# Kernel tuning notes

Hardware: AMD Instinct MI355X
Metric: run time of the kernel (lower is better)

Reference implementation:

```python
import jax, jax.numpy as jnp
import numpy as np

N_NODES = 50000


def _gcn_norm(edge_index, n):
    # Add self-loops (PyG GCNConv default) and compute symmetric normalization.
    src = jnp.concatenate([edge_index[0], jnp.arange(n, dtype=edge_index.dtype)])
    dst = jnp.concatenate([edge_index[1], jnp.arange(n, dtype=edge_index.dtype)])
    deg = jax.ops.segment_sum(jnp.ones(src.shape[0], dtype=jnp.float32), dst,
                              num_segments=n)
    dinv = jnp.where(deg > 0, jax.lax.rsqrt(deg), 0.0)
    norm = dinv[src] * dinv[dst]  # [E+N]
    return src, dst, norm


def _gcn_conv(x, src, dst, norm, W, b, n):
    h = x @ W                              # [N, out] linear transform first
    msgs = h[src] * norm[:, None]          # gather + edge-wise scale [E+N, out]
    out = jax.ops.segment_sum(msgs, dst, num_segments=n)  # scatter-add
    return out + b


def setup_inputs() -> dict:
    key = jax.random.key(0)
    k1, k2, k3, k4 = jax.random.split(key, 4)
    N, E, F, H, C = N_NODES, 1600000, 128, 128, 64
    x = jax.random.normal(k1, (N, F), dtype=jnp.float32)
    edge_index = jax.random.randint(k2, (2, E), 0, N, dtype=jnp.int64)
    W1 = jax.random.normal(k3, (F, H), dtype=jnp.float32) * 0.05
    b1 = jnp.zeros((H,), dtype=jnp.float32)
    W2 = jax.random.normal(k4, (H, C), dtype=jnp.float32) * 0.05
    b2 = jnp.zeros((C,), dtype=jnp.float32)
    return {"x": x, "edge_index": edge_index, "W1": W1, "b1": b1,
            "W2": W2, "b2": b2}


def reference(x, edge_index, W1, b1, W2, b2):
    n = x.shape[0]
    src, dst, norm = _gcn_norm(edge_index, n)
    h = _gcn_conv(x, src, dst, norm, W1, b1, n)
    h = jax.nn.relu(h)
    out = _gcn_conv(h, src, dst, norm, W2, b2, n)
    return out
```

## Files before the change

kernel.cpp:

```cpp
#include <hip/hip_runtime.h>
#include <hip/hip_bf16.h>
#include <stdint.h>

#define N_NODES 50000
#define N_EDGES 1600000
#define N_TOT   (N_EDGES + N_NODES)
#define NBKT      256
#define BKT_NODES 196
#define BKT_CAP   7168
#define TILE      4096
#define EPT       16

typedef unsigned short u16;
typedef __attribute__((ext_vector_type(8))) short short8;
typedef __attribute__((ext_vector_type(4))) float floatx4;

__device__ __forceinline__ float b2f(u16 u) {
    union { unsigned int i; float f; } v; v.i = ((unsigned int)u) << 16; return v.f;
}
__device__ __forceinline__ u16 f2b(float f) {
    union { unsigned int i; float f; } v; v.f = f;
    unsigned int r = (v.i + 0x7FFFu + ((v.i >> 16) & 1u)) >> 16;
    return (u16)r;
}

__global__ void k_detect(const unsigned* __restrict__ xw,
                         const unsigned* __restrict__ ew,
                         int* __restrict__ flags) {
    __shared__ int cnt[2];
    int tid = threadIdx.x;
    if (tid < 2) cnt[tid] = 0;
    __syncthreads();
    unsigned w = xw[tid];
    int e = (w >> 7) & 0xFF;
    int plaus = (e == 0) || (e >= 0x60 && e <= 0x9F);
    unsigned hw = ew[2 * tid + 1];
    atomicAdd(&cnt[0], plaus);
    atomicAdd(&cnt[1], hw == 0 ? 1 : 0);
    __syncthreads();
    if (tid == 0) {
        flags[0] = (cnt[0] < 160) ? 1 : 0;
        flags[1] = (cnt[1] > 250) ? 1 : 0;
    }
}

__global__ void k_zero(int* p) { p[threadIdx.x] = 0; }

__global__ __launch_bounds__(256) void k_part(const int* __restrict__ ei,
                                              const int* __restrict__ flags,
                                              unsigned* __restrict__ pairs,
                                              int* __restrict__ bktcnt) {
    __shared__ unsigned pairsL[TILE];
    __shared__ unsigned char bktL[TILE];
    __shared__ int hist[NBKT], incl[NBKT], delta[NBKT];
    int tid = threadIdx.x;
    long base = (long)blockIdx.x * TILE;
    int i64 = flags[1];
    hist[tid] = 0;
    __syncthreads();

    int myb[EPT], myrank[EPT]; unsigned myp[EPT];
#pragma unroll
    for (int t = 0; t < EPT; t++) {
        long idx = base + t * 256 + tid;
        int b = -1; unsigned p = 0;
        if (idx < N_TOT) {
            int s, d;
            if (idx < N_EDGES) {
                if (i64) { s = ei[2 * idx]; d = ei[2 * (N_EDGES + idx)]; }
                else     { s = ei[idx];     d = ei[N_EDGES + idx]; }
            } else {
                s = d = (int)(idx - N_EDGES);
            }
            b = d / BKT_NODES;
            p = (unsigned)s | ((unsigned)(d - b * BKT_NODES) << 16);
        }
        myb[t] = b; myp[t] = p;
        myrank[t] = (b >= 0) ? atomicAdd(&hist[b], 1) : 0;
    }
    __syncthreads();

    int tot = hist[tid];
    incl[tid] = tot;
    __syncthreads();
    for (int o = 1; o < NBKT; o <<= 1) {
        int t2 = (tid >= o) ? incl[tid - o] : 0;
        __syncthreads();
        incl[tid] += t2;
        __syncthreads();
    }
    int excl = incl[tid] - tot;
    int gb = atomicAdd(&bktcnt[tid], tot);
    hist[tid]  = excl;
    delta[tid] = tid * BKT_CAP + gb - excl;
    __syncthreads();

#pragma unroll
    for (int t = 0; t < EPT; t++) {
        if (myb[t] >= 0) {
            int slot = hist[myb[t]] + myrank[t];
            pairsL[slot] = myp[t];
            bktL[slot]   = (unsigned char)myb[t];
        }
    }
    __syncthreads();
    int count = incl[NBKT - 1];
    for (int i = tid; i < count; i += 256) {
        int b = bktL[i];
        int pos = delta[b] + i;
        if (pos - b * BKT_CAP < BKT_CAP)
            pairs[pos] = pairsL[i];
    }
}

__global__ __launch_bounds__(256) void k_bktscan(const int* __restrict__ bktcnt,
                                                 int* __restrict__ bktbase) {
    __shared__ int s[NBKT];
    int tid = threadIdx.x;
    int v = bktcnt[tid];
    s[tid] = v;
    __syncthreads();
    for (int o = 1; o < NBKT; o <<= 1) {
        int t = (tid >= o) ? s[tid - o] : 0;
        __syncthreads();
        s[tid] += t;
        __syncthreads();
    }
    bktbase[tid] = s[tid] - v;
}

__global__ __launch_bounds__(256) void k_bucket(const unsigned* __restrict__ pairs,
                                                const int* __restrict__ bktcnt,
                                                const int* __restrict__ bktbase,
                                                int* __restrict__ rowstart,
                                                int* __restrict__ deg,
                                                float* __restrict__ dinv,
                                                u16* __restrict__ csr) {
    __shared__ u16 csrL[BKT_CAP];
    __shared__ int degL[NBKT], curL[NBKT], scanT[NBKT];
    int b = blockIdx.x, tid = threadIdx.x;
    int cnt  = bktcnt[b];
    int base = bktbase[b];
    const unsigned* reg = pairs + (size_t)b * BKT_CAP;
    degL[tid] = 0;
    __syncthreads();
    for (int i = tid; i < cnt; i += 256)
        atomicAdd(&degL[reg[i] >> 16], 1);
    __syncthreads();
    int v = degL[tid];
    scanT[tid] = v;
    __syncthreads();
    for (int o = 1; o < NBKT; o <<= 1) {
        int t = (tid >= o) ? scanT[tid - o] : 0;
        __syncthreads();
        scanT[tid] += t;
        __syncthreads();
    }
    int excl = scanT[tid] - v;
    curL[tid] = excl;
    int n = b * BKT_NODES + tid;
    if (tid < BKT_NODES && n < N_NODES) {
        rowstart[n] = base + excl;
        deg[n]      = v;
        dinv[n]     = rsqrtf((float)v);
    }
    __syncthreads();
    for (int i = tid; i < cnt; i += 256) {
        unsigned p = reg[i];
        int slot = atomicAdd(&curL[p >> 16], 1);
        csrL[slot] = (u16)(p & 0xFFFFu);
    }
    __syncthreads();
    for (int i = tid; i < cnt; i += 256)
        csr[base + i] = csrL[i];
}

template<int NOUT, bool ADYN>
__global__ __launch_bounds__(256) void k_gemm(const void* __restrict__ A,
                                              const void* __restrict__ W,
                                              u16* __restrict__ out, int M,
                                              const int* __restrict__ flags) {
    const int isf32 = flags[0];
    constexpr int LDW = 136;
    __shared__ __align__(16) u16 Wt[NOUT * LDW];
    int tid = threadIdx.x;
    const float* Wf = (const float*)W;
    const u16*   Wu = (const u16*)W;
    for (int idx = tid; idx < 128 * NOUT; idx += 256) {
        int k = idx / NOUT, n = idx % NOUT;
        Wt[n * LDW + k] = isf32 ? f2b(Wf[idx]) : Wu[idx];
    }
    __syncthreads();

    int wave = tid >> 6, lane = tid & 63;
    int quad = lane >> 4, l16 = lane & 15;
    int r0 = blockIdx.x * 64 + wave * 16;
    int r = r0 + l16; if (r >= M) r = M - 1;

    floatx4 acc[NOUT / 16];
#pragma unroll
    for (int i = 0; i < NOUT / 16; i++) acc[i] = (floatx4)(0.f);

#pragma unroll
    for (int ks = 0; ks < 4; ks++) {
        short8 a;
        if (ADYN && isf32) {
            const float* af = (const float*)A + (size_t)r * 128 + ks * 32 + quad * 8;
            float4 v0 = ((const float4*)af)[0];
            float4 v1 = ((const float4*)af)[1];
            a[0] = (short)f2b(v0.x); a[1] = (short)f2b(v0.y);
            a[2] = (short)f2b(v0.z); a[3] = (short)f2b(v0.w);
            a[4] = (short)f2b(v1.x); a[5] = (short)f2b(v1.y);
            a[6] = (short)f2b(v1.z); a[7] = (short)f2b(v1.w);
        } else {
            a = ((const short8*)((const u16*)A + (size_t)r * 128))[ks * 4 + quad];
        }
#pragma unroll
        for (int nt = 0; nt < NOUT / 16; nt++) {
            const short8* bp = (const short8*)&Wt[(nt * 16 + l16) * LDW + ks * 32 + quad * 8];
            acc[nt] = __builtin_amdgcn_mfma_f32_16x16x32_bf16(a, *bp, acc[nt], 0, 0, 0);
        }
    }
#pragma unroll
    for (int nt = 0; nt < NOUT / 16; nt++) {
#pragma unroll
        for (int j = 0; j < 4; j++) {
            int row = r0 + quad * 4 + j;
            if (row < M) out[(size_t)row * NOUT + nt * 16 + l16] = f2b(acc[nt][j]);
        }
    }
}

__global__ __launch_bounds__(256) void k_agg1(const u16* __restrict__ h,
                                              const u16* __restrict__ csr,
                                              const int* __restrict__ rowstart,
                                              const int* __restrict__ deg,
                                              const float* __restrict__ dinv,
                                              const void* __restrict__ bias,
                                              u16* __restrict__ out,
                                              const int* __restrict__ flags) {
    int wave = threadIdx.x >> 6, lane = threadIdx.x & 63;
    int d = blockIdx.x * 4 + wave;
    if (d >= N_NODES) return;
    int quad = lane >> 4, l16 = lane & 15;
    int start = rowstart[d], end = start + deg[d];
    float dd = dinv[d];
    float acc[8] = {0.f, 0.f, 0.f, 0.f, 0.f, 0.f, 0.f, 0.f};
    for (int e = start + quad; e < end; e += 4) {
        int s = csr[e];
        float w = dinv[s] * dd;
        uint4 v = ((const uint4*)(h + (size_t)s * 128))[l16];
        acc[0] += w * b2f(v.x & 0xFFFF); acc[1] += w * b2f(v.x >> 16);
        acc[2] += w * b2f(v.y & 0xFFFF); acc[3] += w * b2f(v.y >> 16);
        acc[4] += w * b2f(v.z & 0xFFFF); acc[5] += w * b2f(v.z >> 16);
        acc[6] += w * b2f(v.w & 0xFFFF); acc[7] += w * b2f(v.w >> 16);
    }
#pragma unroll
    for (int j = 0; j < 8; j++) {
        acc[j] += __shfl_xor(acc[j], 16);
        acc[j] += __shfl_xor(acc[j], 32);
    }
    if (quad == 0) {
        int isf32 = flags[0];
        u16 r[8];
#pragma unroll
        for (int j = 0; j < 8; j++) {
            float bv = isf32 ? ((const float*)bias)[l16 * 8 + j]
                             : b2f(((const u16*)bias)[l16 * 8 + j]);
            float v = acc[j] + bv;
            r[j] = f2b(v > 0.f ? v : 0.f);
        }
        uint4 o;
        o.x = r[0] | ((unsigned)r[1] << 16); o.y = r[2] | ((unsigned)r[3] << 16);
        o.z = r[4] | ((unsigned)r[5] << 16); o.w = r[6] | ((unsigned)r[7] << 16);
        ((uint4*)(out + (size_t)d * 128))[l16] = o;
    }
}

__global__ __launch_bounds__(256) void k_agg2(const u16* __restrict__ h,
                                              const u16* __restrict__ csr,
                                              const int* __restrict__ rowstart,
                                              const int* __restrict__ deg,
                                              const float* __restrict__ dinv,
                                              const void* __restrict__ bias,
                                              float* __restrict__ out,
                                              const int* __restrict__ flags) {
    int wave = threadIdx.x >> 6, lane = threadIdx.x & 63;
    int d = blockIdx.x * 4 + wave;
    if (d >= N_NODES) return;
    int oct = lane >> 3, l8 = lane & 7;
    int start = rowstart[d], end = start + deg[d];
    float dd = dinv[d];
    float acc[8] = {0.f, 0.f, 0.f, 0.f, 0.f, 0.f, 0.f, 0.f};
    for (int e = start + oct; e < end; e += 8) {
        int s = csr[e];
        float w = dinv[s] * dd;
        uint4 v = ((const uint4*)(h + (size_t)s * 64))[l8];
        acc[0] += w * b2f(v.x & 0xFFFF); acc[1] += w * b2f(v.x >> 16);
        acc[2] += w * b2f(v.y & 0xFFFF); acc[3] += w * b2f(v.y >> 16);
        acc[4] += w * b2f(v.z & 0xFFFF); acc[5] += w * b2f(v.z >> 16);
        acc[6] += w * b2f(v.w & 0xFFFF); acc[7] += w * b2f(v.w >> 16);
    }
#pragma unroll
    for (int j = 0; j < 8; j++) {
        acc[j] += __shfl_xor(acc[j], 8);
        acc[j] += __shfl_xor(acc[j], 16);
        acc[j] += __shfl_xor(acc[j], 32);
    }
    if (oct == 0) {
        int isf32 = flags[0];
        float r[8];
#pragma unroll
        for (int j = 0; j < 8; j++) {
            float bv = isf32 ? ((const float*)bias)[l8 * 8 + j]
                             : b2f(((const u16*)bias)[l8 * 8 + j]);
            r[j] = acc[j] + bv;
        }
        float4 oa, ob;
        oa.x = r[0]; oa.y = r[1]; oa.z = r[2]; oa.w = r[3];
        ob.x = r[4]; ob.y = r[5]; ob.z = r[6]; ob.w = r[7];
        ((float4*)(out + (size_t)d * 64))[l8 * 2]     = oa;
        ((float4*)(out + (size_t)d * 64))[l8 * 2 + 1] = ob;
    }
}

extern "C" void kernel_launch(void* const* d_in, const int* in_sizes, int n_in,
                              void* d_out, int out_size, void* d_ws, size_t ws_size,
                              hipStream_t stream) {
    const void* x  = d_in[0];
    const int*  ei = (const int*)d_in[1];
    const void* W1 = d_in[2];
    const void* b1 = d_in[3];
    const void* W2 = d_in[4];
    const void* b2 = d_in[5];
    float* out = (float*)d_out;

    char* ws = (char*)d_ws;
    int*      flags    = (int*)(ws + 0);
    int*      bktcnt   = (int*)(ws + 1024);
    int*      bktbase  = (int*)(ws + 2048);
    int*      deg      = (int*)(ws + 4096);
    int*      rowstart = (int*)(ws + 204800);
    float*    dinv     = (float*)(ws + 405504);
    unsigned* pairs    = (unsigned*)(ws + 606208);
    u16*      csr      = (u16*)(ws + 7946240);
    u16*      h1       = (u16*)(ws + 11247616);
    u16*      out1     = (u16*)(ws + 24047616);
    u16*      h2       = h1;

    k_detect <<<1, 256, 0, stream>>>((const unsigned*)x, (const unsigned*)ei, flags);
    k_zero   <<<1, 256, 0, stream>>>(bktcnt);
    k_part   <<<(N_TOT + TILE - 1) / TILE, 256, 0, stream>>>(ei, flags, pairs, bktcnt);
    k_bktscan<<<1, 256, 0, stream>>>(bktcnt, bktbase);
    k_bucket <<<NBKT, 256, 0, stream>>>(pairs, bktcnt, bktbase, rowstart, deg, dinv, csr);

    k_gemm<128, true> <<<(N_NODES + 63) / 64, 256, 0, stream>>>(x, W1, h1, N_NODES, flags);
    k_agg1<<<(N_NODES + 3) / 4, 256, 0, stream>>>(h1, csr, rowstart, deg, dinv, b1, out1, flags);
    k_gemm<64, false> <<<(N_NODES + 63) / 64, 256, 0, stream>>>(out1, W2, h2, N_NODES, flags);
    k_agg2<<<(N_NODES + 3) / 4, 256, 0, stream>>>(h2, csr, rowstart, deg, dinv, b2, out, flags);
}
```

Baseline: 290.4 us.

## Fold source-degree scaling into GEMM epilogue and widen aggregation lanes

The GEMM epilogue now multiplies each output row by dinv[row], so the aggregation kernels no longer gather dinv[src] per edge. They apply the destination dinv once at the end instead. The aggregation kernels give each lane 16 features instead of 8, process two edges per iteration with more edges in flight, and reduce with an extra shuffle stage. The zero-init kernel is merged into the detect kernel to save one launch. This trades a per-edge random load and multiply for a slightly different rounding order, since the pre-scaled values are stored in bf16.

```diff
diff --git a/kernel.cpp b/kernel.cpp
--- a/kernel.cpp
+++ b/kernel.cpp
@@ -26,9 +26,11 @@
 
 __global__ void k_detect(const unsigned* __restrict__ xw,
                          const unsigned* __restrict__ ew,
-                         int* __restrict__ flags) {
+                         int* __restrict__ flags,
+                         int* __restrict__ bktcnt) {
     __shared__ int cnt[2];
     int tid = threadIdx.x;
+    bktcnt[tid] = 0;
     if (tid < 2) cnt[tid] = 0;
     __syncthreads();
     unsigned w = xw[tid];
@@ -43,8 +45,6 @@
         flags[1] = (cnt[1] > 250) ? 1 : 0;
     }
 }
-
-__global__ void k_zero(int* p) { p[threadIdx.x] = 0; }
 
 __global__ __launch_bounds__(256) void k_part(const int* __restrict__ ei,
                                               const int* __restrict__ flags,
@@ -178,6 +178,7 @@
 template<int NOUT, bool ADYN>
 __global__ __launch_bounds__(256) void k_gemm(const void* __restrict__ A,
                                               const void* __restrict__ W,
+                                              const float* __restrict__ dinv,
                                               u16* __restrict__ out, int M,
                                               const int* __restrict__ flags) {
     const int isf32 = flags[0];
@@ -221,12 +222,18 @@
             acc[nt] = __builtin_amdgcn_mfma_f32_16x16x32_bf16(a, *bp, acc[nt], 0, 0, 0);
         }
     }
+    float sc[4];
+#pragma unroll
+    for (int j = 0; j < 4; j++) {
+        int row = r0 + quad * 4 + j;
+        sc[j] = dinv[row < M ? row : 0];
+    }
 #pragma unroll
     for (int nt = 0; nt < NOUT / 16; nt++) {
 #pragma unroll
         for (int j = 0; j < 4; j++) {
             int row = r0 + quad * 4 + j;
-            if (row < M) out[(size_t)row * NOUT + nt * 16 + l16] = f2b(acc[nt][j]);
+            if (row < M) out[(size_t)row * NOUT + nt * 16 + l16] = f2b(acc[nt][j] * sc[j]);
         }
     }
 }
@@ -242,38 +249,73 @@
     int wave = threadIdx.x >> 6, lane = threadIdx.x & 63;
     int d = blockIdx.x * 4 + wave;
     if (d >= N_NODES) return;
-    int quad = lane >> 4, l16 = lane & 15;
+    int oct = lane >> 3, l8 = lane & 7;
     int start = rowstart[d], end = start + deg[d];
-    float dd = dinv[d];
-    float acc[8] = {0.f, 0.f, 0.f, 0.f, 0.f, 0.f, 0.f, 0.f};
-    for (int e = start + quad; e < end; e += 4) {
-        int s = csr[e];
-        float w = dinv[s] * dd;
-        uint4 v = ((const uint4*)(h + (size_t)s * 128))[l16];
-        acc[0] += w * b2f(v.x & 0xFFFF); acc[1] += w * b2f(v.x >> 16);
-        acc[2] += w * b2f(v.y & 0xFFFF); acc[3] += w * b2f(v.y >> 16);
-        acc[4] += w * b2f(v.z & 0xFFFF); acc[5] += w * b2f(v.z >> 16);
-        acc[6] += w * b2f(v.w & 0xFFFF); acc[7] += w * b2f(v.w >> 16);
-    }
-#pragma unroll
-    for (int j = 0; j < 8; j++) {
+    float acc[16];
+#pragma unroll
+    for (int j = 0; j < 16; j++) acc[j] = 0.f;
+
+    int e = start + oct;
+    for (; e + 8 < end; e += 16) {
+        int s0 = csr[e], s1 = csr[e + 8];
+        const uint4* p0 = (const uint4*)(h + (size_t)s0 * 128);
+        const uint4* p1 = (const uint4*)(h + (size_t)s1 * 128);
+        uint4 a0 = p0[l8 * 2], b0 = p0[l8 * 2 + 1];
+        uint4 a1 = p1[l8 * 2], b1 = p1[l8 * 2 + 1];
+        acc[0]  += b2f(a0.x & 0xFFFF); acc[1]  += b2f(a0.x >> 16);
+        acc[2]  += b2f(a0.y & 0xFFFF); acc[3]  += b2f(a0.y >> 16);
+        acc[4]  += b2f(a0.z & 0xFFFF); acc[5]  += b2f(a0.z >> 16);
+        acc[6]  += b2f(a0.w & 0xFFFF); acc[7]  += b2f(a0.w >> 16);
+        acc[8]  += b2f(b0.x & 0xFFFF); acc[9]  += b2f(b0.x >> 16);
+        acc[10] += b2f(b0.y & 0xFFFF); acc[11] += b2f(b0.y >> 16);
+        acc[12] += b2f(b0.z & 0xFFFF); acc[13] += b2f(b0.z >> 16);
+        acc[14] += b2f(b0.w & 0xFFFF); acc[15] += b2f(b0.w >> 16);
+        acc[0]  += b2f(a1.x & 0xFFFF); acc[1]  += b2f(a1.x >> 16);
+        acc[2]  += b2f(a1.y & 0xFFFF); acc[3]  += b2f(a1.y >> 16);
+        acc[4]  += b2f(a1.z & 0xFFFF); acc[5]  += b2f(a1.z >> 16);
+        acc[6]  += b2f(a1.w & 0xFFFF); acc[7]  += b2f(a1.w >> 16);
+        acc[8]  += b2f(b1.x & 0xFFFF); acc[9]  += b2f(b1.x >> 16);
+        acc[10] += b2f(b1.y & 0xFFFF); acc[11] += b2f(b1.y >> 16);
+        acc[12] += b2f(b1.z & 0xFFFF); acc[13] += b2f(b1.z >> 16);
+        acc[14] += b2f(b1.w & 0xFFFF); acc[15] += b2f(b1.w >> 16);
+    }
+    if (e < end) {
+        int s0 = csr[e];
+        const uint4* p0 = (const uint4*)(h + (size_t)s0 * 128);
+        uint4 a0 = p0[l8 * 2], b0 = p0[l8 * 2 + 1];
+        acc[0]  += b2f(a0.x & 0xFFFF); acc[1]  += b2f(a0.x >> 16);
+        acc[2]  += b2f(a0.y & 0xFFFF); acc[3]  += b2f(a0.y >> 16);
+        acc[4]  += b2f(a0.z & 0xFFFF); acc[5]  += b2f(a0.z >> 16);
+        acc[6]  += b2f(a0.w & 0xFFFF); acc[7]  += b2f(a0.w >> 16);
+        acc[8]  += b2f(b0.x & 0xFFFF); acc[9]  += b2f(b0.x >> 16);
+        acc[10] += b2f(b0.y & 0xFFFF); acc[11] += b2f(b0.y >> 16);
+        acc[12] += b2f(b0.z & 0xFFFF); acc[13] += b2f(b0.z >> 16);
+        acc[14] += b2f(b0.w & 0xFFFF); acc[15] += b2f(b0.w >> 16);
+    }
+#pragma unroll
+    for (int j = 0; j < 16; j++) {
+        acc[j] += __shfl_xor(acc[j], 8);
         acc[j] += __shfl_xor(acc[j], 16);
         acc[j] += __shfl_xor(acc[j], 32);
     }
-    if (quad == 0) {
+    if (oct == 0) {
         int isf32 = flags[0];
-        u16 r[8];
-#pragma unroll
-        for (int j = 0; j < 8; j++) {
-            float bv = isf32 ? ((const float*)bias)[l16 * 8 + j]
-                             : b2f(((const u16*)bias)[l16 * 8 + j]);
-            float v = acc[j] + bv;
+        float dd = dinv[d];
+        u16 r[16];
+#pragma unroll
+        for (int j = 0; j < 16; j++) {
+            float bv = isf32 ? ((const float*)bias)[l8 * 16 + j]
+                             : b2f(((const u16*)bias)[l8 * 16 + j]);
+            float v = acc[j] * dd + bv;
             r[j] = f2b(v > 0.f ? v : 0.f);
         }
-        uint4 o;
-        o.x = r[0] | ((unsigned)r[1] << 16); o.y = r[2] | ((unsigned)r[3] << 16);
-        o.z = r[4] | ((unsigned)r[5] << 16); o.w = r[6] | ((unsigned)r[7] << 16);
-        ((uint4*)(out + (size_t)d * 128))[l16] = o;
+        uint4 o0, o1;
+        o0.x = r[0] | ((unsigned)r[1] << 16);  o0.y = r[2] | ((unsigned)r[3] << 16);
+        o0.z = r[4] | ((unsigned)r[5] << 16);  o0.w = r[6] | ((unsigned)r[7] << 16);
+        o1.x = r[8] | ((unsigned)r[9] << 16);  o1.y = r[10] | ((unsigned)r[11] << 16);
+        o1.z = r[12] | ((unsigned)r[13] << 16); o1.w = r[14] | ((unsigned)r[15] << 16);
+        ((uint4*)(out + (size_t)d * 128))[l8 * 2]     = o0;
+        ((uint4*)(out + (size_t)d * 128))[l8 * 2 + 1] = o1;
     }
 }
 
@@ -288,39 +330,71 @@
     int wave = threadIdx.x >> 6, lane = threadIdx.x & 63;
     int d = blockIdx.x * 4 + wave;
     if (d >= N_NODES) return;
-    int oct = lane >> 3, l8 = lane & 7;
+    int grp = lane >> 2, l4 = lane & 3;
     int start = rowstart[d], end = start + deg[d];
-    float dd = dinv[d];
-    float acc[8] = {0.f, 0.f, 0.f, 0.f, 0.f, 0.f, 0.f, 0.f};
-    for (int e = start + oct; e < end; e += 8) {
-        int s = csr[e];
-        float w = dinv[s] * dd;
-        uint4 v = ((const uint4*)(h + (size_t)s * 64))[l8];
-        acc[0] += w * b2f(v.x & 0xFFFF); acc[1] += w * b2f(v.x >> 16);
-        acc[2] += w * b2f(v.y & 0xFFFF); acc[3] += w * b2f(v.y >> 16);
-        acc[4] += w * b2f(v.z & 0xFFFF); acc[5] += w * b2f(v.z >> 16);
-        acc[6] += w * b2f(v.w & 0xFFFF); acc[7] += w * b2f(v.w >> 16);
-    }
-#pragma unroll
-    for (int j = 0; j < 8; j++) {
+    float acc[16];
+#pragma unroll
+    for (int j = 0; j < 16; j++) acc[j] = 0.f;
+
+    int e = start + grp;
+    for (; e + 16 < end; e += 32) {
+        int s0 = csr[e], s1 = csr[e + 16];
+        const uint4* p0 = (const uint4*)(h + (size_t)s0 * 64);
+        const uint4* p1 = (const uint4*)(h + (size_t)s1 * 64);
+        uint4 a0 = p0[l4 * 2], b0 = p0[l4 * 2 + 1];
+        uint4 a1 = p1[l4 * 2], b1 = p1[l4 * 2 + 1];
+        acc[0]  += b2f(a0.x & 0xFFFF); acc[1]  += b2f(a0.x >> 16);
+        acc[2]  += b2f(a0.y & 0xFFFF); acc[3]  += b2f(a0.y >> 16);
+        acc[4]  += b2f(a0.z & 0xFFFF); acc[5]  += b2f(a0.z >> 16);
+        acc[6]  += b2f(a0.w & 0xFFFF); acc[7]  += b2f(a0.w >> 16);
+        acc[8]  += b2f(b0.x & 0xFFFF); acc[9]  += b2f(b0.x >> 16);
+        acc[10] += b2f(b0.y & 0xFFFF); acc[11] += b2f(b0.y >> 16);
+        acc[12] += b2f(b0.z & 0xFFFF); acc[13] += b2f(b0.z >> 16);
+        acc[14] += b2f(b0.w & 0xFFFF); acc[15] += b2f(b0.w >> 16);
+        acc[0]  += b2f(a1.x & 0xFFFF); acc[1]  += b2f(a1.x >> 16);
+        acc[2]  += b2f(a1.y & 0xFFFF); acc[3]  += b2f(a1.y >> 16);
+        acc[4]  += b2f(a1.z & 0xFFFF); acc[5]  += b2f(a1.z >> 16);
+        acc[6]  += b2f(a1.w & 0xFFFF); acc[7]  += b2f(a1.w >> 16);
+        acc[8]  += b2f(b1.x & 0xFFFF); acc[9]  += b2f(b1.x >> 16);
+        acc[10] += b2f(b1.y & 0xFFFF); acc[11] += b2f(b1.y >> 16);
+        acc[12] += b2f(b1.z & 0xFFFF); acc[13] += b2f(b1.z >> 16);
+        acc[14] += b2f(b1.w & 0xFFFF); acc[15] += b2f(b1.w >> 16);
+    }
+    if (e < end) {
+        int s0 = csr[e];
+        const uint4* p0 = (const uint4*)(h + (size_t)s0 * 64);
+        uint4 a0 = p0[l4 * 2], b0 = p0[l4 * 2 + 1];
+        acc[0]  += b2f(a0.x & 0xFFFF); acc[1]  += b2f(a0.x >> 16);
+        acc[2]  += b2f(a0.y & 0xFFFF); acc[3]  += b2f(a0.y >> 16);
+        acc[4]  += b2f(a0.z & 0xFFFF); acc[5]  += b2f(a0.z >> 16);
+        acc[6]  += b2f(a0.w & 0xFFFF); acc[7]  += b2f(a0.w >> 16);
+        acc[8]  += b2f(b0.x & 0xFFFF); acc[9]  += b2f(b0.x >> 16);
+        acc[10] += b2f(b0.y & 0xFFFF); acc[11] += b2f(b0.y >> 16);
+        acc[12] += b2f(b0.z & 0xFFFF); acc[13] += b2f(b0.z >> 16);
+        acc[14] += b2f(b0.w & 0xFFFF); acc[15] += b2f(b0.w >> 16);
+    }
+#pragma unroll
+    for (int j = 0; j < 16; j++) {
+        acc[j] += __shfl_xor(acc[j], 4);
         acc[j] += __shfl_xor(acc[j], 8);
         acc[j] += __shfl_xor(acc[j], 16);
         acc[j] += __shfl_xor(acc[j], 32);
     }
-    if (oct == 0) {
+    if (grp == 0) {
         int isf32 = flags[0];
-        float r[8];
-#pragma unroll
-        for (int j = 0; j < 8; j++) {
-            float bv = isf32 ? ((const float*)bias)[l8 * 8 + j]
-                             : b2f(((const u16*)bias)[l8 * 8 + j]);
-            r[j] = acc[j] + bv;
-        }
-        float4 oa, ob;
-        oa.x = r[0]; oa.y = r[1]; oa.z = r[2]; oa.w = r[3];
-        ob.x = r[4]; ob.y = r[5]; ob.z = r[6]; ob.w = r[7];
-        ((float4*)(out + (size_t)d * 64))[l8 * 2]     = oa;
-        ((float4*)(out + (size_t)d * 64))[l8 * 2 + 1] = ob;
+        float dd = dinv[d];
+        float r[16];
+#pragma unroll
+        for (int j = 0; j < 16; j++) {
+            float bv = isf32 ? ((const float*)bias)[l4 * 16 + j]
+                             : b2f(((const u16*)bias)[l4 * 16 + j]);
+            r[j] = acc[j] * dd + bv;
+        }
+        float4* op = (float4*)(out + (size_t)d * 64) + l4 * 4;
+        op[0] = make_float4(r[0],  r[1],  r[2],  r[3]);
+        op[1] = make_float4(r[4],  r[5],  r[6],  r[7]);
+        op[2] = make_float4(r[8],  r[9],  r[10], r[11]);
+        op[3] = make_float4(r[12], r[13], r[14], r[15]);
     }
 }
 
@@ -348,14 +422,13 @@
     u16*      out1     = (u16*)(ws + 24047616);
     u16*      h2       = h1;
 
-    k_detect <<<1, 256, 0, stream>>>((const unsigned*)x, (const unsigned*)ei, flags);
-    k_zero   <<<1, 256, 0, stream>>>(bktcnt);
+    k_detect <<<1, 256, 0, stream>>>((const unsigned*)x, (const unsigned*)ei, flags, bktcnt);
     k_part   <<<(N_TOT + TILE - 1) / TILE, 256, 0, stream>>>(ei, flags, pairs, bktcnt);
     k_bktscan<<<1, 256, 0, stream>>>(bktcnt, bktbase);
     k_bucket <<<NBKT, 256, 0, stream>>>(pairs, bktcnt, bktbase, rowstart, deg, dinv, csr);
 
-    k_gemm<128, true> <<<(N_NODES + 63) / 64, 256, 0, stream>>>(x, W1, h1, N_NODES, flags);
+    k_gemm<128, true> <<<(N_NODES + 63) / 64, 256, 0, stream>>>(x, W1, dinv, h1, N_NODES, flags);
     k_agg1<<<(N_NODES + 3) / 4, 256, 0, stream>>>(h1, csr, rowstart, deg, dinv, b1, out1, flags);
-    k_gemm<64, false> <<<(N_NODES + 63) / 64, 256, 0, stream>>>(out1, W2, h2, N_NODES, flags);
+    k_gemm<64, false> <<<(N_NODES + 63) / 64, 256, 0, stream>>>(out1, W2, dinv, h2, N_NODES, flags);
     k_agg2<<<(N_NODES + 3) / 4, 256, 0, stream>>>(h2, csr, rowstart, deg, dinv, b2, out, flags);
 }
```

After: 261.2 us. 1.11x faster.

## Fold source-degree scaling into GEMM epilogue and unroll aggregation gathers

Applied to the files above, without the earlier changes.

The GEMM epilogue now multiplies each output row by dinv[row], so the aggregation kernels no longer read dinv[s] per edge. The destination dinv is applied once after the reduction. Both aggregation kernels use 8 lanes per edge and a 4-way unrolled gather to keep more loads in flight, accumulating into packed float2 values. The zeroing kernel is merged into k_detect to save a launch. Rounding changes slightly because h is scaled before the bf16 cast.

```diff
diff --git a/kernel.cpp b/kernel.cpp
--- a/kernel.cpp
+++ b/kernel.cpp
@@ -18,6 +18,9 @@
 __device__ __forceinline__ float b2f(u16 u) {
     union { unsigned int i; float f; } v; v.i = ((unsigned int)u) << 16; return v.f;
 }
+__device__ __forceinline__ float asf(unsigned u) {
+    union { unsigned int i; float f; } v; v.i = u; return v.f;
+}
 __device__ __forceinline__ u16 f2b(float f) {
     union { unsigned int i; float f; } v; v.f = f;
     unsigned int r = (v.i + 0x7FFFu + ((v.i >> 16) & 1u)) >> 16;
@@ -26,9 +29,11 @@
 
 __global__ void k_detect(const unsigned* __restrict__ xw,
                          const unsigned* __restrict__ ew,
-                         int* __restrict__ flags) {
+                         int* __restrict__ flags,
+                         int* __restrict__ bktcnt) {
     __shared__ int cnt[2];
     int tid = threadIdx.x;
+    bktcnt[tid] = 0;
     if (tid < 2) cnt[tid] = 0;
     __syncthreads();
     unsigned w = xw[tid];
@@ -43,8 +48,6 @@
         flags[1] = (cnt[1] > 250) ? 1 : 0;
     }
 }
-
-__global__ void k_zero(int* p) { p[threadIdx.x] = 0; }
 
 __global__ __launch_bounds__(256) void k_part(const int* __restrict__ ei,
                                               const int* __restrict__ flags,
@@ -178,6 +181,7 @@
 template<int NOUT, bool ADYN>
 __global__ __launch_bounds__(256) void k_gemm(const void* __restrict__ A,
                                               const void* __restrict__ W,
+                                              const float* __restrict__ dinv,
                                               u16* __restrict__ out, int M,
                                               const int* __restrict__ flags) {
     const int isf32 = flags[0];
@@ -221,15 +225,23 @@
             acc[nt] = __builtin_amdgcn_mfma_f32_16x16x32_bf16(a, *bp, acc[nt], 0, 0, 0);
         }
     }
+    float sc[4];
+#pragma unroll
+    for (int j = 0; j < 4; j++) {
+        int row = r0 + quad * 4 + j;
+        sc[j] = dinv[row < M ? row : 0];
+    }
 #pragma unroll
     for (int nt = 0; nt < NOUT / 16; nt++) {
 #pragma unroll
         for (int j = 0; j < 4; j++) {
             int row = r0 + quad * 4 + j;
-            if (row < M) out[(size_t)row * NOUT + nt * 16 + l16] = f2b(acc[nt][j]);
-        }
-    }
-}
+            if (row < M) out[(size_t)row * NOUT + nt * 16 + l16] = f2b(acc[nt][j] * sc[j]);
+        }
+    }
+}
+
+#define ACCU(u, j) { acc[j].x += asf((u) << 16); acc[j].y += asf((u) & 0xFFFF0000u); }
 
 __global__ __launch_bounds__(256) void k_agg1(const u16* __restrict__ h,
                                               const u16* __restrict__ csr,
@@ -242,38 +254,67 @@
     int wave = threadIdx.x >> 6, lane = threadIdx.x & 63;
     int d = blockIdx.x * 4 + wave;
     if (d >= N_NODES) return;
-    int quad = lane >> 4, l16 = lane & 15;
+    int oct = lane >> 3, l8 = lane & 7;
     int start = rowstart[d], end = start + deg[d];
-    float dd = dinv[d];
-    float acc[8] = {0.f, 0.f, 0.f, 0.f, 0.f, 0.f, 0.f, 0.f};
-    for (int e = start + quad; e < end; e += 4) {
-        int s = csr[e];
-        float w = dinv[s] * dd;
-        uint4 v = ((const uint4*)(h + (size_t)s * 128))[l16];
-        acc[0] += w * b2f(v.x & 0xFFFF); acc[1] += w * b2f(v.x >> 16);
-        acc[2] += w * b2f(v.y & 0xFFFF); acc[3] += w * b2f(v.y >> 16);
-        acc[4] += w * b2f(v.z & 0xFFFF); acc[5] += w * b2f(v.z >> 16);
-        acc[6] += w * b2f(v.w & 0xFFFF); acc[7] += w * b2f(v.w >> 16);
+    float2 acc[8];
+#pragma unroll
+    for (int j = 0; j < 8; j++) acc[j] = make_float2(0.f, 0.f);
+
+    int e = start + oct;
+    for (; e + 24 < end; e += 32) {
+        int s0 = csr[e], s1 = csr[e + 8], s2 = csr[e + 16], s3 = csr[e + 24];
+        const uint4* p0 = (const uint4*)(h + (size_t)s0 * 128) + l8 * 2;
+        const uint4* p1 = (const uint4*)(h + (size_t)s1 * 128) + l8 * 2;
+        const uint4* p2 = (const uint4*)(h + (size_t)s2 * 128) + l8 * 2;
+        const uint4* p3 = (const uint4*)(h + (size_t)s3 * 128) + l8 * 2;
+        uint4 a0 = p0[0], b0 = p0[1];
+        uint4 a1 = p1[0], b1 = p1[1];
+        uint4 a2 = p2[0], b2 = p2[1];
+        uint4 a3 = p3[0], b3 = p3[1];
+        ACCU(a0.x,0) ACCU(a0.y,1) ACCU(a0.z,2) ACCU(a0.w,3)
+        ACCU(b0.x,4) ACCU(b0.y,5) ACCU(b0.z,6) ACCU(b0.w,7)
+        ACCU(a1.x,0) ACCU(a1.y,1) ACCU(a1.z,2) ACCU(a1.w,3)
+        ACCU(b1.x,4) ACCU(b1.y,5) ACCU(b1.z,6) ACCU(b1.w,7)
+        ACCU(a2.x,0) ACCU(a2.y,1) ACCU(a2.z,2) ACCU(a2.w,3)
+        ACCU(b2.x,4) ACCU(b2.y,5) ACCU(b2.z,6) ACCU(b2.w,7)
+        ACCU(a3.x,0) ACCU(a3.y,1) ACCU(a3.z,2) ACCU(a3.w,3)
+        ACCU(b3.x,4) ACCU(b3.y,5) ACCU(b3.z,6) ACCU(b3.w,7)
+    }
+    for (; e < end; e += 8) {
+        int s0 = csr[e];
+        const uint4* p0 = (const uint4*)(h + (size_t)s0 * 128) + l8 * 2;
+        uint4 a0 = p0[0], b0 = p0[1];
+        ACCU(a0.x,0) ACCU(a0.y,1) ACCU(a0.z,2) ACCU(a0.w,3)
+        ACCU(b0.x,4) ACCU(b0.y,5) ACCU(b0.z,6) ACCU(b0.w,7)
     }
 #pragma unroll
     for (int j = 0; j < 8; j++) {
-        acc[j] += __shfl_xor(acc[j], 16);
-        acc[j] += __shfl_xor(acc[j], 32);
-    }
-    if (quad == 0) {
+        acc[j].x += __shfl_xor(acc[j].x, 8);  acc[j].y += __shfl_xor(acc[j].y, 8);
+        acc[j].x += __shfl_xor(acc[j].x, 16); acc[j].y += __shfl_xor(acc[j].y, 16);
+        acc[j].x += __shfl_xor(acc[j].x, 32); acc[j].y += __shfl_xor(acc[j].y, 32);
+    }
+    if (oct == 0) {
         int isf32 = flags[0];
-        u16 r[8];
+        float dd = dinv[d];
+        u16 r[16];
 #pragma unroll
         for (int j = 0; j < 8; j++) {
-            float bv = isf32 ? ((const float*)bias)[l16 * 8 + j]
-                             : b2f(((const u16*)bias)[l16 * 8 + j]);
-            float v = acc[j] + bv;
-            r[j] = f2b(v > 0.f ? v : 0.f);
-        }
-        uint4 o;
-        o.x = r[0] | ((unsigned)r[1] << 16); o.y = r[2] | ((unsigned)r[3] << 16);
-        o.z = r[4] | ((unsigned)r[5] << 16); o.w = r[6] | ((unsigned)r[7] << 16);
-        ((uint4*)(out + (size_t)d * 128))[l16] = o;
+            float bx = isf32 ? ((const float*)bias)[l8 * 16 + 2 * j]
+                             : b2f(((const u16*)bias)[l8 * 16 + 2 * j]);
+            float by = isf32 ? ((const float*)bias)[l8 * 16 + 2 * j + 1]
+                             : b2f(((const u16*)bias)[l8 * 16 + 2 * j + 1]);
+            float vx = acc[j].x * dd + bx;
+            float vy = acc[j].y * dd + by;
+            r[2 * j]     = f2b(vx > 0.f ? vx : 0.f);
+            r[2 * j + 1] = f2b(vy > 0.f ? vy : 0.f);
+        }
+        uint4 o0, o1;
+        o0.x = r[0] | ((unsigned)r[1] << 16);  o0.y = r[2] | ((unsigned)r[3] << 16);
+        o0.z = r[4] | ((unsigned)r[5] << 16);  o0.w = r[6] | ((unsigned)r[7] << 16);
+        o1.x = r[8] | ((unsigned)r[9] << 16);  o1.y = r[10] | ((unsigned)r[11] << 16);
+        o1.z = r[12] | ((unsigned)r[13] << 16); o1.w = r[14] | ((unsigned)r[15] << 16);
+        ((uint4*)(out + (size_t)d * 128))[l8 * 2]     = o0;
+        ((uint4*)(out + (size_t)d * 128))[l8 * 2 + 1] = o1;
     }
 }
 
@@ -290,37 +331,49 @@
     if (d >= N_NODES) return;
     int oct = lane >> 3, l8 = lane & 7;
     int start = rowstart[d], end = start + deg[d];
-    float dd = dinv[d];
-    float acc[8] = {0.f, 0.f, 0.f, 0.f, 0.f, 0.f, 0.f, 0.f};
-    for (int e = start + oct; e < end; e += 8) {
-        int s = csr[e];
-        float w = dinv[s] * dd;
-        uint4 v = ((const uint4*)(h + (size_t)s * 64))[l8];
-        acc[0] += w * b2f(v.x & 0xFFFF); acc[1] += w * b2f(v.x >> 16);
-        acc[2] += w * b2f(v.y & 0xFFFF); acc[3] += w * b2f(v.y >> 16);
-        acc[4] += w * b2f(v.z & 0xFFFF); acc[5] += w * b2f(v.z >> 16);
-        acc[6] += w * b2f(v.w & 0xFFFF); acc[7] += w * b2f(v.w >> 16);
-    }
-#pragma unroll
-    for (int j = 0; j < 8; j++) {
-        acc[j] += __shfl_xor(acc[j], 8);
-        acc[j] += __shfl_xor(acc[j], 16);
-        acc[j] += __shfl_xor(acc[j], 32);
+    float2 acc[4];
+#pragma unroll
+    for (int j = 0; j < 4; j++) acc[j] = make_float2(0.f, 0.f);
+
+    int e = start + oct;
+    for (; e + 24 < end; e += 32) {
+        int s0 = csr[e], s1 = csr[e + 8], s2 = csr[e + 16], s3 = csr[e + 24];
+        uint4 v0 = ((const uint4*)(h + (size_t)s0 * 64))[l8];
+        uint4 v1 = ((const uint4*)(h + (size_t)s1 * 64))[l8];
+        uint4 v2 = ((const uint4*)(h + (size_t)s2 * 64))[l8];
+        uint4 v3 = ((const uint4*)(h + (size_t)s3 * 64))[l8];
+        ACCU(v0.x,0) ACCU(v0.y,1) ACCU(v0.z,2) ACCU(v0.w,3)
+        ACCU(v1.x,0) ACCU(v1.y,1) ACCU(v1.z,2) ACCU(v1.w,3)
+        ACCU(v2.x,0) ACCU(v2.y,1) ACCU(v2.z,2) ACCU(v2.w,3)
+        ACCU(v3.x,0) ACCU(v3.y,1) ACCU(v3.z,2) ACCU(v3.w,3)
+    }
+    for (; e < end; e += 8) {
+        int s0 = csr[e];
+        uint4 v0 = ((const uint4*)(h + (size_t)s0 * 64))[l8];
+        ACCU(v0.x,0) ACCU(v0.y,1) ACCU(v0.z,2) ACCU(v0.w,3)
+    }
+#pragma unroll
+    for (int j = 0; j < 4; j++) {
+        acc[j].x += __shfl_xor(acc[j].x, 8);  acc[j].y += __shfl_xor(acc[j].y, 8);
+        acc[j].x += __shfl_xor(acc[j].x, 16); acc[j].y += __shfl_xor(acc[j].y, 16);
+        acc[j].x += __shfl_xor(acc[j].x, 32); acc[j].y += __shfl_xor(acc[j].y, 32);
     }
     if (oct == 0) {
         int isf32 = flags[0];
+        float dd = dinv[d];
         float r[8];
 #pragma unroll
-        for (int j = 0; j < 8; j++) {
-            float bv = isf32 ? ((const float*)bias)[l8 * 8 + j]
-                             : b2f(((const u16*)bias)[l8 * 8 + j]);
-            r[j] = acc[j] + bv;
-        }
-        float4 oa, ob;
-        oa.x = r[0]; oa.y = r[1]; oa.z = r[2]; oa.w = r[3];
-        ob.x = r[4]; ob.y = r[5]; ob.z = r[6]; ob.w = r[7];
-        ((float4*)(out + (size_t)d * 64))[l8 * 2]     = oa;
-        ((float4*)(out + (size_t)d * 64))[l8 * 2 + 1] = ob;
+        for (int j = 0; j < 4; j++) {
+            float bx = isf32 ? ((const float*)bias)[l8 * 8 + 2 * j]
+                             : b2f(((const u16*)bias)[l8 * 8 + 2 * j]);
+            float by = isf32 ? ((const float*)bias)[l8 * 8 + 2 * j + 1]
+                             : b2f(((const u16*)bias)[l8 * 8 + 2 * j + 1]);
+            r[2 * j]     = acc[j].x * dd + bx;
+            r[2 * j + 1] = acc[j].y * dd + by;
+        }
+        float4* op = (float4*)(out + (size_t)d * 64) + l8 * 2;
+        op[0] = make_float4(r[0], r[1], r[2], r[3]);
+        op[1] = make_float4(r[4], r[5], r[6], r[7]);
     }
 }
 
@@ -348,14 +401,13 @@
     u16*      out1     = (u16*)(ws + 24047616);
     u16*      h2       = h1;
 
-    k_detect <<<1, 256, 0, stream>>>((const unsigned*)x, (const unsigned*)ei, flags);
-    k_zero   <<<1, 256, 0, stream>>>(bktcnt);
+    k_detect <<<1, 256, 0, stream>>>((const unsigned*)x, (const unsigned*)ei, flags, bktcnt);
     k_part   <<<(N_TOT + TILE - 1) / TILE, 256, 0, stream>>>(ei, flags, pairs, bktcnt);
     k_bktscan<<<1, 256, 0, stream>>>(bktcnt, bktbase);
     k_bucket <<<NBKT, 256, 0, stream>>>(pairs, bktcnt, bktbase, rowstart, deg, dinv, csr);
 
-    k_gemm<128, true> <<<(N_NODES + 63) / 64, 256, 0, stream>>>(x, W1, h1, N_NODES, flags);
+    k_gemm<128, true> <<<(N_NODES + 63) / 64, 256, 0, stream>>>(x, W1, dinv, h1, N_NODES, flags);
     k_agg1<<<(N_NODES + 3) / 4, 256, 0, stream>>>(h1, csr, rowstart, deg, dinv, b1, out1, flags);
-    k_gemm<64, false> <<<(N_NODES + 63) / 64, 256, 0, stream>>>(out1, W2, h2, N_NODES, flags);
+    k_gemm<64, false> <<<(N_NODES + 63) / 64, 256, 0, stream>>>(out1, W2, dinv, h2, N_NODES, flags);
     k_agg2<<<(N_NODES + 3) / 4, 256, 0, stream>>>(h2, csr, rowstart, deg, dinv, b2, out, flags);
 }
```

Measured after the change: 255.6 us. 1.14x faster.
